# Kernel optimization log

Measured on AMD Instinct MI355X. Metric: run time of the kernel, lower is better.

Reference implementation:

```python
import jax, jax.numpy as jnp
import numpy as np


def setup_inputs() -> dict:
    key = jax.random.key(0)
    k1, k2, k3, k4 = jax.random.split(key, 4)
    B, T, d_model, d_internal = 4, 2048, 1024, 64
    x = jax.random.normal(k1, (B, T, d_model), dtype=jnp.float32)
    # torch.nn.Linear weights: [out_features, in_features]
    s = 1.0 / np.sqrt(d_model)
    W_Q = jax.random.uniform(k2, (d_internal, d_model), jnp.float32, -s, s)
    W_K = jax.random.uniform(k3, (d_internal, d_model), jnp.float32, -s, s)
    W_V = jax.random.uniform(k4, (d_internal, d_model), jnp.float32, -s, s)
    return {"x": x, "W_Q": W_Q, "W_K": W_K, "W_V": W_V}


def reference(x, W_Q, W_K, W_V):
    B, T, C = x.shape  # C == d_model
    Q = jnp.einsum('btc,dc->btd', x, W_Q)
    K = jnp.einsum('btc,dc->btd', x, W_K)
    # Faithful to source bug: V is computed with W_K, W_V is unused.
    V = jnp.einsum('btc,dc->btd', x, W_K)
    scale = C ** (-0.5)  # source scales by d_model, not d_internal
    attn = jnp.einsum('btd,bsd->bts', Q, K) * scale  # [B,T,T]
    causal = jnp.tril(jnp.ones((T, T), dtype=bool))
    attn = jnp.where(causal[None, :, :], attn, -jnp.inf)
    attn = jax.nn.softmax(attn, axis=-1)
    return jnp.einsum('bts,bsd->btd', attn, V)
```

## Files before the change

### kernel.cpp

```cpp
#include <hip/hip_runtime.h>
#include <hip/hip_bf16.h>
#include <cstdint>
#include <cstddef>

#define BB 4
#define TT 2048
#define DM 1024
#define DH 64

typedef __attribute__((ext_vector_type(8))) short short8;
typedef __attribute__((ext_vector_type(4))) float floatx4;

__device__ __forceinline__ unsigned short f2bf(float f) {
    union { float f; unsigned int u; } v; v.f = f;
    unsigned int u = v.u;
    u += 0x7fffu + ((u >> 16) & 1u);
    return (unsigned short)(u >> 16);
}

#define XTHREADS (512 * 32 * 64)
#define WTHREADS (8 * 32 * 64)

__global__ __launch_bounds__(256) void conv_kernel(const float* __restrict__ x,
                                                   const float* __restrict__ wq,
                                                   const float* __restrict__ wk,
                                                   unsigned short* __restrict__ xbt,
                                                   unsigned short* __restrict__ wbt) {
    const int t = blockIdx.x * 256 + threadIdx.x;
    const float* src;
    unsigned short* dst;
    if (t < XTHREADS) {
        const int l  = t & 63;
        const int kc = (t >> 6) & 31;
        const int mt = t >> 11;
        src = x + (size_t)(mt * 16 + (l & 15)) * DM + kc * 32 + (l >> 4) * 8;
        dst = xbt + (size_t)t * 8;
    } else {
        const int j  = t - XTHREADS;
        const int l  = j & 63;
        const int kc = (j >> 6) & 31;
        const int nt = j >> 11;
        const float* wbase = (nt < 4) ? wq : wk;
        const int    row   = (nt & 3) * 16 + (l & 15);
        src = wbase + (size_t)row * DM + kc * 32 + (l >> 4) * 8;
        dst = wbt + (size_t)j * 8;
    }
    float4 a = *reinterpret_cast<const float4*>(src);
    float4 b = *reinterpret_cast<const float4*>(src + 4);
    short8 r;
    r[0] = (short)f2bf(a.x); r[1] = (short)f2bf(a.y);
    r[2] = (short)f2bf(a.z); r[3] = (short)f2bf(a.w);
    r[4] = (short)f2bf(b.x); r[5] = (short)f2bf(b.y);
    r[6] = (short)f2bf(b.z); r[7] = (short)f2bf(b.w);
    *reinterpret_cast<short8*>(dst) = r;
}

__global__ __launch_bounds__(256, 4) void proj_kernel(const unsigned short* __restrict__ xbt,
                                                      const unsigned short* __restrict__ wbt,
                                                      unsigned short* __restrict__ qo,
                                                      unsigned short* __restrict__ ko,
                                                      unsigned short* __restrict__ kt) {
    const int tid  = threadIdx.x;
    const int wave = tid >> 6;
    const int lane = tid & 63;
    const int col  = lane & 15;
    const int quad = lane >> 4;
    const int mt   = blockIdx.x >> 1;
    const int half = blockIdx.x & 1;
    const int nt   = half * 4 + wave;

    const unsigned short* ap = xbt + ((size_t)mt * 32 * 64 + lane) * 8;
    const unsigned short* bp = wbt + ((size_t)nt * 32 * 64 + lane) * 8;

    floatx4 acc = (floatx4){0.f, 0.f, 0.f, 0.f};
#pragma unroll 8
    for (int kc = 0; kc < 32; ++kc) {
        short8 a = *reinterpret_cast<const short8*>(ap + (size_t)kc * 512);
        short8 b = *reinterpret_cast<const short8*>(bp + (size_t)kc * 512);
        acc = __builtin_amdgcn_mfma_f32_16x16x32_bf16(a, b, acc, 0, 0, 0);
    }

    const int g = wave * 16 + col;
#pragma unroll
    for (int r = 0; r < 4; ++r) {
        const size_t row = (size_t)(mt * 16 + quad * 4 + r);
        if (half == 0) {
            qo[row * DH + g] = f2bf(acc[r] * 0.03125f);
        } else {
            unsigned short h = f2bf(acc[r]);
            ko[row * DH + g] = h;
            const int b4 = (int)(row >> 11);
            const int s  = (int)(row & 2047);
            kt[((size_t)(b4 * 64 + g)) * TT + s] = h;
        }
    }
}

__global__ __launch_bounds__(128) void flash1_kernel(const unsigned short* __restrict__ qb,
                                                     const unsigned short* __restrict__ kb,
                                                     const unsigned short* __restrict__ ktb,
                                                     float* __restrict__ Op,
                                                     float* __restrict__ ml) {
    const int c  = blockIdx.x & 15;
    const int qt = (blockIdx.x >> 4) & 63;
    const int b  = blockIdx.x >> 10;
    if (4 * c > qt) return;

    __shared__ __align__(16) unsigned short Pl[2][16][40];

    const int tid  = threadIdx.x;
    const int wave = tid >> 6;
    const int lane = tid & 63;
    const int col  = lane & 15;
    const int quad = lane >> 4;

    const int q0    = qt * 32;
    const int qrow  = q0 + wave * 16;
    const int s_beg = c * 128;
    const int s_end = min(s_beg + 128, q0 + 32);

    const unsigned short* qp  = qb  + ((size_t)b * TT + qrow) * DH;
    const unsigned short* kp  = kb  + (size_t)b * TT * DH;
    const unsigned short* ktp = ktb + (size_t)b * 64 * TT;

    short8 qf0 = *reinterpret_cast<const short8*>(qp + (size_t)col * DH + quad * 8);
    short8 qf1 = *reinterpret_cast<const short8*>(qp + (size_t)col * DH + 32 + quad * 8);

    floatx4 o[4];
#pragma unroll
    for (int t = 0; t < 4; ++t) o[t] = (floatx4){0.f, 0.f, 0.f, 0.f};
    float lrow[4] = {0.f, 0.f, 0.f, 0.f};
    int   myq[4];
#pragma unroll
    for (int r = 0; r < 4; ++r) myq[r] = qrow + quad * 4 + r;
    const float LOG2E = 1.44269504f;

    for (int s0 = s_beg; s0 < s_end; s0 += 32) {
        float sv[2][4];
#pragma unroll
        for (int st = 0; st < 2; ++st) {
            const unsigned short* kr = kp + (size_t)(s0 + st * 16 + col) * DH + quad * 8;
            short8 kf0 = *reinterpret_cast<const short8*>(kr);
            short8 kf1 = *reinterpret_cast<const short8*>(kr + 32);
            floatx4 z = (floatx4){0.f, 0.f, 0.f, 0.f};
            z = __builtin_amdgcn_mfma_f32_16x16x32_bf16(qf0, kf0, z, 0, 0, 0);
            z = __builtin_amdgcn_mfma_f32_16x16x32_bf16(qf1, kf1, z, 0, 0, 0);
            const int skey = s0 + st * 16 + col;
#pragma unroll
            for (int r = 0; r < 4; ++r) {
                float p = __builtin_exp2f(z[r] * LOG2E);
                p = (skey <= myq[r]) ? p : 0.f;
                sv[st][r] = p;
                lrow[r] += p;
            }
        }

#pragma unroll
        for (int st = 0; st < 2; ++st)
#pragma unroll
            for (int r = 0; r < 4; ++r)
                Pl[wave][quad * 4 + r][st * 16 + col] = f2bf(sv[st][r]);
        short8 pf = *reinterpret_cast<const short8*>(&Pl[wave][col][quad * 8]);

#pragma unroll
        for (int t = 0; t < 4; ++t) {
            short8 vf = *reinterpret_cast<const short8*>(
                ktp + (size_t)(t * 16 + col) * TT + s0 + quad * 8);
            o[t] = __builtin_amdgcn_mfma_f32_16x16x32_bf16(pf, vf, o[t], 0, 0, 0);
        }
    }

#pragma unroll
    for (int m = 1; m < 16; m <<= 1)
#pragma unroll
        for (int r = 0; r < 4; ++r)
            lrow[r] += __shfl_xor(lrow[r], m, 64);

    const int slot = (b * 64 + qt) * 16 + c;
    float* op = Op + (size_t)slot * 2048;
#pragma unroll
    for (int t = 0; t < 4; ++t)
#pragma unroll
        for (int r = 0; r < 4; ++r)
            op[(size_t)(wave * 16 + quad * 4 + r) * DH + t * 16 + col] = o[t][r];
    if (col == 0) {
        float* mlp = ml + (size_t)slot * 32;
#pragma unroll
        for (int r = 0; r < 4; ++r)
            mlp[wave * 16 + quad * 4 + r] = lrow[r];
    }
}

__global__ __launch_bounds__(256) void merge_kernel(const float* __restrict__ Op,
                                                    const float* __restrict__ ml,
                                                    float* __restrict__ out) {
    const int qt  = blockIdx.x & 63;
    const int b   = blockIdx.x >> 6;
    const int nch = (qt >> 2) + 1;
    const int t   = threadIdx.x;
    const int row = t >> 3;
    const int c8  = (t & 7) * 8;
    const size_t base = (size_t)blockIdx.x * 16;

    float L = 0.f;
    float a[8];
#pragma unroll
    for (int i = 0; i < 8; ++i) a[i] = 0.f;
#pragma unroll 4
    for (int c = 0; c < nch; ++c) {
        L += ml[(base + c) * 32 + row];
        const float* op = Op + (base + c) * 2048 + (size_t)row * 64 + c8;
        float4 v0 = *reinterpret_cast<const float4*>(op);
        float4 v1 = *reinterpret_cast<const float4*>(op + 4);
        a[0] += v0.x; a[1] += v0.y; a[2] += v0.z; a[3] += v0.w;
        a[4] += v1.x; a[5] += v1.y; a[6] += v1.z; a[7] += v1.w;
    }
    const float inv = 1.0f / L;
    float* o = out + ((size_t)b * TT + qt * 32 + row) * DH + c8;
    float4 r0 = {a[0] * inv, a[1] * inv, a[2] * inv, a[3] * inv};
    float4 r1 = {a[4] * inv, a[5] * inv, a[6] * inv, a[7] * inv};
    *reinterpret_cast<float4*>(o)     = r0;
    *reinterpret_cast<float4*>(o + 4) = r1;
}

extern "C" void kernel_launch(void* const* d_in, const int* in_sizes, int n_in,
                              void* d_out, int out_size, void* d_ws, size_t ws_size,
                              hipStream_t stream) {
    const float* x  = (const float*)d_in[0];
    const float* wq = (const float*)d_in[1];
    const float* wk = (const float*)d_in[2];

    unsigned short* xbt = (unsigned short*)d_ws;
    unsigned short* wbt = xbt + (size_t)XTHREADS * 8;
    unsigned short* qo  = wbt + (size_t)WTHREADS * 8;
    unsigned short* ko  = qo + (size_t)BB * TT * DH;
    unsigned short* kt  = ko + (size_t)BB * TT * DH;
    float* Op = (float*)(kt + (size_t)BB * DH * TT);
    float* ml = Op + (size_t)4096 * 2048;
    float* out = (float*)d_out;

    const int conv_blocks = (XTHREADS + WTHREADS) / 256;
    hipLaunchKernelGGL(conv_kernel,   dim3(conv_blocks),  dim3(256), 0, stream, x, wq, wk, xbt, wbt);
    hipLaunchKernelGGL(proj_kernel,   dim3(1024),         dim3(256), 0, stream, xbt, wbt, qo, ko, kt);
    hipLaunchKernelGGL(flash1_kernel, dim3(BB * 64 * 16), dim3(128), 0, stream, qo, ko, kt, Op, ml);
    hipLaunchKernelGGL(merge_kernel,  dim3(BB * 64),      dim3(256), 0, stream, Op, ml, out);
}
```

Measured before the change: 131.5 us.

## Fuse x bf16 conversion into projection kernel and coalesce transposed K stores

Result: faster. 126.7 us (-3.7%).

```diff
diff --git a/kernel.cpp b/kernel.cpp
--- a/kernel.cpp
+++ b/kernel.cpp
@@ -18,81 +18,96 @@
     return (unsigned short)(u >> 16);
 }
 
-#define XTHREADS (512 * 32 * 64)
+__device__ __forceinline__ short8 cvt8(float4 lo, float4 hi) {
+    short8 r;
+    r[0] = (short)f2bf(lo.x); r[1] = (short)f2bf(lo.y);
+    r[2] = (short)f2bf(lo.z); r[3] = (short)f2bf(lo.w);
+    r[4] = (short)f2bf(hi.x); r[5] = (short)f2bf(hi.y);
+    r[6] = (short)f2bf(hi.z); r[7] = (short)f2bf(hi.w);
+    return r;
+}
+
 #define WTHREADS (8 * 32 * 64)
 
-__global__ __launch_bounds__(256) void conv_kernel(const float* __restrict__ x,
-                                                   const float* __restrict__ wq,
-                                                   const float* __restrict__ wk,
-                                                   unsigned short* __restrict__ xbt,
-                                                   unsigned short* __restrict__ wbt) {
-    const int t = blockIdx.x * 256 + threadIdx.x;
-    const float* src;
-    unsigned short* dst;
-    if (t < XTHREADS) {
-        const int l  = t & 63;
-        const int kc = (t >> 6) & 31;
-        const int mt = t >> 11;
-        src = x + (size_t)(mt * 16 + (l & 15)) * DM + kc * 32 + (l >> 4) * 8;
-        dst = xbt + (size_t)t * 8;
-    } else {
-        const int j  = t - XTHREADS;
-        const int l  = j & 63;
-        const int kc = (j >> 6) & 31;
-        const int nt = j >> 11;
-        const float* wbase = (nt < 4) ? wq : wk;
-        const int    row   = (nt & 3) * 16 + (l & 15);
-        src = wbase + (size_t)row * DM + kc * 32 + (l >> 4) * 8;
-        dst = wbt + (size_t)j * 8;
-    }
+__global__ __launch_bounds__(256) void wtile_kernel(const float* __restrict__ wq,
+                                                    const float* __restrict__ wk,
+                                                    unsigned short* __restrict__ wbt) {
+    const int j  = blockIdx.x * 256 + threadIdx.x;
+    const int l  = j & 63;
+    const int kc = (j >> 6) & 31;
+    const int nt = j >> 11;
+    const float* wbase = (nt < 4) ? wq : wk;
+    const float* src = wbase + (size_t)((nt & 3) * 16 + (l & 15)) * DM
+                             + kc * 32 + (l >> 4) * 8;
     float4 a = *reinterpret_cast<const float4*>(src);
     float4 b = *reinterpret_cast<const float4*>(src + 4);
-    short8 r;
-    r[0] = (short)f2bf(a.x); r[1] = (short)f2bf(a.y);
-    r[2] = (short)f2bf(a.z); r[3] = (short)f2bf(a.w);
-    r[4] = (short)f2bf(b.x); r[5] = (short)f2bf(b.y);
-    r[6] = (short)f2bf(b.z); r[7] = (short)f2bf(b.w);
-    *reinterpret_cast<short8*>(dst) = r;
-}
-
-__global__ __launch_bounds__(256, 4) void proj_kernel(const unsigned short* __restrict__ xbt,
-                                                      const unsigned short* __restrict__ wbt,
-                                                      unsigned short* __restrict__ qo,
-                                                      unsigned short* __restrict__ ko,
-                                                      unsigned short* __restrict__ kt) {
+    *reinterpret_cast<short8*>(wbt + (size_t)j * 8) = cvt8(a, b);
+}
+
+__global__ __launch_bounds__(256) void proj_kernel(const float* __restrict__ x,
+                                                   const unsigned short* __restrict__ wbt,
+                                                   unsigned short* __restrict__ qo,
+                                                   unsigned short* __restrict__ ko,
+                                                   unsigned short* __restrict__ kt) {
+    __shared__ __align__(16) unsigned short sA[32 * 64 * 8];
+
     const int tid  = threadIdx.x;
     const int wave = tid >> 6;
     const int lane = tid & 63;
     const int col  = lane & 15;
     const int quad = lane >> 4;
-    const int mt   = blockIdx.x >> 1;
-    const int half = blockIdx.x & 1;
-    const int nt   = half * 4 + wave;
-
-    const unsigned short* ap = xbt + ((size_t)mt * 32 * 64 + lane) * 8;
-    const unsigned short* bp = wbt + ((size_t)nt * 32 * 64 + lane) * 8;
-
-    floatx4 acc = (floatx4){0.f, 0.f, 0.f, 0.f};
+    const int mt   = blockIdx.x;
+
+    const float* xtile = x + (size_t)mt * 16 * DM;
+#pragma unroll 8
+    for (int i = 0; i < 8; ++i) {
+        const int e  = tid + i * 256;
+        const int kc = e >> 6;
+        const int l  = e & 63;
+        const float* src = xtile + (size_t)(l & 15) * DM + kc * 32 + (l >> 4) * 8;
+        float4 a = *reinterpret_cast<const float4*>(src);
+        float4 b = *reinterpret_cast<const float4*>(src + 4);
+        *reinterpret_cast<short8*>(sA + (size_t)e * 8) = cvt8(a, b);
+    }
+    __syncthreads();
+
+    const unsigned short* bq = wbt + ((size_t)wave * 32 * 64) * 8;
+    const unsigned short* bk = wbt + ((size_t)(4 + wave) * 32 * 64) * 8;
+
+    floatx4 accQ = (floatx4){0.f, 0.f, 0.f, 0.f};
+    floatx4 accK = (floatx4){0.f, 0.f, 0.f, 0.f};
 #pragma unroll 8
     for (int kc = 0; kc < 32; ++kc) {
-        short8 a = *reinterpret_cast<const short8*>(ap + (size_t)kc * 512);
-        short8 b = *reinterpret_cast<const short8*>(bp + (size_t)kc * 512);
-        acc = __builtin_amdgcn_mfma_f32_16x16x32_bf16(a, b, acc, 0, 0, 0);
+        short8 a  = *reinterpret_cast<const short8*>(sA + ((size_t)kc * 64 + lane) * 8);
+        short8 b0 = *reinterpret_cast<const short8*>(bq + ((size_t)kc * 64 + lane) * 8);
+        short8 b1 = *reinterpret_cast<const short8*>(bk + ((size_t)kc * 64 + lane) * 8);
+        accQ = __builtin_amdgcn_mfma_f32_16x16x32_bf16(a, b0, accQ, 0, 0, 0);
+        accK = __builtin_amdgcn_mfma_f32_16x16x32_bf16(a, b1, accK, 0, 0, 0);
     }
 
     const int g = wave * 16 + col;
+    unsigned short hk[4];
 #pragma unroll
     for (int r = 0; r < 4; ++r) {
         const size_t row = (size_t)(mt * 16 + quad * 4 + r);
-        if (half == 0) {
-            qo[row * DH + g] = f2bf(acc[r] * 0.03125f);
-        } else {
-            unsigned short h = f2bf(acc[r]);
-            ko[row * DH + g] = h;
-            const int b4 = (int)(row >> 11);
-            const int s  = (int)(row & 2047);
-            kt[((size_t)(b4 * 64 + g)) * TT + s] = h;
-        }
+        qo[row * DH + g] = f2bf(accQ[r] * 0.03125f);
+        hk[r] = f2bf(accK[r]);
+        ko[row * DH + g] = hk[r];
+    }
+
+    __syncthreads();
+    unsigned short* kts = sA;
+#pragma unroll
+    for (int r = 0; r < 4; ++r)
+        kts[g * 16 + quad * 4 + r] = hk[r];
+    __syncthreads();
+    if (tid < 128) {
+        const int d  = tid >> 1;
+        const int s8 = (tid & 1) * 8;
+        const int b4 = mt >> 7;
+        const int s0 = (mt & 127) * 16 + s8;
+        short8 v = *reinterpret_cast<const short8*>(kts + d * 16 + s8);
+        *reinterpret_cast<short8*>(kt + ((size_t)(b4 * 64 + d)) * TT + s0) = v;
     }
 }
 
@@ -106,7 +121,7 @@
     const int b  = blockIdx.x >> 10;
     if (4 * c > qt) return;
 
-    __shared__ __align__(16) unsigned short Pl[2][16][40];
+    __shared__ __align__(16) unsigned short Pl[2][2][16][40];
 
     const int tid  = threadIdx.x;
     const int wave = tid >> 6;
@@ -135,7 +150,7 @@
     for (int r = 0; r < 4; ++r) myq[r] = qrow + quad * 4 + r;
     const float LOG2E = 1.44269504f;
 
-    for (int s0 = s_beg; s0 < s_end; s0 += 32) {
+    auto body = [&](int s0, int slot) {
         float sv[2][4];
 #pragma unroll
         for (int st = 0; st < 2; ++st) {
@@ -154,13 +169,12 @@
                 lrow[r] += p;
             }
         }
-
 #pragma unroll
         for (int st = 0; st < 2; ++st)
 #pragma unroll
             for (int r = 0; r < 4; ++r)
-                Pl[wave][quad * 4 + r][st * 16 + col] = f2bf(sv[st][r]);
-        short8 pf = *reinterpret_cast<const short8*>(&Pl[wave][col][quad * 8]);
+                Pl[wave][slot][quad * 4 + r][st * 16 + col] = f2bf(sv[st][r]);
+        short8 pf = *reinterpret_cast<const short8*>(&Pl[wave][slot][col][quad * 8]);
 
 #pragma unroll
         for (int t = 0; t < 4; ++t) {
@@ -168,6 +182,14 @@
                 ktp + (size_t)(t * 16 + col) * TT + s0 + quad * 8);
             o[t] = __builtin_amdgcn_mfma_f32_16x16x32_bf16(pf, vf, o[t], 0, 0, 0);
         }
+    };
+
+    const int nIter = (s_end - s_beg) >> 5;
+    if (nIter == 4) {
+        body(s_beg, 0); body(s_beg + 32, 1);
+        body(s_beg + 64, 0); body(s_beg + 96, 1);
+    } else {
+        for (int i = 0; i < nIter; ++i) body(s_beg + 32 * i, i & 1);
     }
 
 #pragma unroll
@@ -230,8 +252,7 @@
     const float* wq = (const float*)d_in[1];
     const float* wk = (const float*)d_in[2];
 
-    unsigned short* xbt = (unsigned short*)d_ws;
-    unsigned short* wbt = xbt + (size_t)XTHREADS * 8;
+    unsigned short* wbt = (unsigned short*)d_ws;
     unsigned short* qo  = wbt + (size_t)WTHREADS * 8;
     unsigned short* ko  = qo + (size_t)BB * TT * DH;
     unsigned short* kt  = ko + (size_t)BB * TT * DH;
@@ -239,9 +260,8 @@
     float* ml = Op + (size_t)4096 * 2048;
     float* out = (float*)d_out;
 
-    const int conv_blocks = (XTHREADS + WTHREADS) / 256;
-    hipLaunchKernelGGL(conv_kernel,   dim3(conv_blocks),  dim3(256), 0, stream, x, wq, wk, xbt, wbt);
-    hipLaunchKernelGGL(proj_kernel,   dim3(1024),         dim3(256), 0, stream, xbt, wbt, qo, ko, kt);
-    hipLaunchKernelGGL(flash1_kernel, dim3(BB * 64 * 16), dim3(128), 0, stream, qo, ko, kt, Op, ml);
-    hipLaunchKernelGGL(merge_kernel,  dim3(BB * 64),      dim3(256), 0, stream, Op, ml, out);
-}
+    hipLaunchKernelGGL(wtile_kernel,  dim3(WTHREADS / 256), dim3(256), 0, stream, wq, wk, wbt);
+    hipLaunchKernelGGL(proj_kernel,   dim3((BB * TT) / 16), dim3(256), 0, stream, x, wbt, qo, ko, kt);
+    hipLaunchKernelGGL(flash1_kernel, dim3(BB * 64 * 16),   dim3(128), 0, stream, qo, ko, kt, Op, ml);
+    hipLaunchKernelGGL(merge_kernel,  dim3(BB * 64),        dim3(256), 0, stream, Op, ml, out);
+}
```
